# Kernel tuning notes

Measured on AMD Instinct MI355X. Metric: run time of the kernel, lower is better.

The kernel has to match this reference:

```python
import jax, jax.numpy as jnp
import numpy as np
from jax import lax

ORI = 256.0  # original image size hardcoded in feature_align
CIN  = [3, 64, 64, 128, 128, 256, 256, 256, 512, 512, 512]
COUT = [64, 64, 128, 128, 256, 256, 256, 512, 512, 512, 512]


def _conv(x, w, b):
    y = lax.conv_general_dilated(x, w, (1, 1), 'SAME',
                                 dimension_numbers=('NCHW', 'OIHW', 'NCHW'))
    return y + b[None, :, None, None]


def _pool(x):
    return lax.reduce_window(x, -jnp.inf, lax.max, (1, 1, 2, 2), (1, 1, 2, 2), 'VALID')


def _vgg(x, ws, bs):
    cr = lambda h, i: jax.nn.relu(_conv(h, ws[i], bs[i]))
    h = cr(x, 0); h = cr(h, 1); h = _pool(h)          # block1
    h = cr(h, 2); h = cr(h, 3); h = _pool(h)          # block2
    h = cr(h, 4); h = cr(h, 5); h = cr(h, 6); h = _pool(h)  # block3
    h = cr(h, 7); h = cr(h, 8); F = h                 # idx 20: relu(conv4_2)
    h = cr(h, 9); h = _pool(h)                        # conv4_3 + pool4
    U = cr(h, 10)                                     # idx 25: relu(conv5_1)
    return F, U


def _interp(im, px, py):
    # im: [C,H,W]; px,py: [n] point coords in original 256x256 space
    C, H, W = im.shape
    step = ORI / H  # feature maps are square (H==W)
    x = (px - step / 2) / ORI * H
    y = (py - step / 2) / ORI * W
    x0f = jnp.floor(x); y0f = jnp.floor(y)
    x0 = jnp.clip(x0f, 0, W - 1).astype(jnp.int32)
    x1 = jnp.clip(x0f + 1, 0, W - 1).astype(jnp.int32)
    y0 = jnp.clip(y0f, 0, H - 1).astype(jnp.int32)
    y1 = jnp.clip(y0f + 1, 0, H - 1).astype(jnp.int32)
    Ia = im[:, y0, x0]; Ib = im[:, y1, x0]; Ic = im[:, y0, x1]; Id = im[:, y1, x1]  # [C,n]
    # boundary weight adjustment, faithful to original scalar code
    xe = x0 == x1; ye = y0 == y1
    x0w = jnp.where(xe & (x0 == 0), x0 - 1, x0).astype(im.dtype)
    x1w = jnp.where(xe & (x0 != 0), x1 + 1, x1).astype(im.dtype)
    y0w = jnp.where(ye & (y0 == 0), y0 - 1, y0).astype(im.dtype)
    y1w = jnp.where(ye & (y0 != 0), y1 + 1, y1).astype(im.dtype)
    wa = (x1w - x) * (y1w - y); wb = (x1w - x) * (y - y0w)
    wc = (x - x0w) * (y1w - y); wd = (x - x0w) * (y - y0w)
    return Ia * wa + Ib * wb + Ic * wc + Id * wd  # [C,n]


def _feature_align(feat, P, mask):
    ns = jnp.sum(mask, axis=1)  # [B] valid point counts
    out = jax.vmap(_interp)(feat, P[..., 0], P[..., 1])  # [B,C,n]
    valid = (jnp.arange(P.shape[1])[None, :] < ns[:, None]).astype(feat.dtype)
    return out * valid[:, None, :]


def setup_inputs() -> dict:
    key = jax.random.key(0)
    ks = jax.random.split(key, 3 + 2 * len(CIN))
    inp = {
        'x': jax.random.normal(ks[0], (8, 3, 256, 256), dtype=jnp.float32),
        'points': jax.random.uniform(ks[1], (8, 32, 2), dtype=jnp.float32,
                                     minval=0.0, maxval=256.0),
        'mask': jnp.ones((8, 32), dtype=jnp.int32),
    }
    for i, (ci, co) in enumerate(zip(CIN, COUT)):
        std = np.sqrt(2.0 / (ci * 9))
        inp[f'w{i}'] = jax.random.normal(ks[2 + 2 * i], (co, ci, 3, 3), dtype=jnp.float32) * std
        inp[f'b{i}'] = jax.random.normal(ks[3 + 2 * i], (co,), dtype=jnp.float32) * 0.01
    return inp


def reference(x, points, mask,
              w0, b0, w1, b1, w2, b2, w3, b3, w4, b4, w5, b5,
              w6, b6, w7, b7, w8, b8, w9, b9, w10, b10):
    ws = [w0, w1, w2, w3, w4, w5, w6, w7, w8, w9, w10]
    bs = [b0, b1, b2, b3, b4, b5, b6, b7, b8, b9, b10]
    Fmap, Umap = _vgg(x, ws, bs)
    F = _feature_align(Fmap, points, mask)  # [B,512,n]
    U = _feature_align(Umap, points, mask)
    return F.transpose(0, 2, 1), U.transpose(0, 2, 1)
```

## Files before the change

### kernel.cpp

```cpp
#include <hip/hip_runtime.h>
#include <cstdint>

template <int CIS, int COB>
__global__ __launch_bounds__(256, 4) void conv1_k(
    const float* __restrict__ in, const float* __restrict__ wgt,
    const float* __restrict__ bias, float* __restrict__ out,
    int Cin, int Cout, int H, int W)
{
    const int tilesX = W >> 4;
    const int tx = blockIdx.x % tilesX;
    const int ty = blockIdx.x / tilesX;
    const int x0 = tx << 4, y0 = ty << 4;
    const int co0 = blockIdx.y * COB;
    const int n = blockIdx.z;
    in  += (size_t)n * Cin * H * W;
    out += (size_t)n * Cout * H * W;

    __shared__ float tile[CIS][18][20];
    __shared__ float wlds[CIS][COB][12];

    const int tid = threadIdx.x;
    const int lx = tid & 15, ly = tid >> 4;
    const int ox = x0 + lx, oy = y0 + ly;

    float acc[COB];
#pragma unroll
    for (int i = 0; i < COB; ++i) acc[i] = 0.f;

    for (int ci0 = 0; ci0 < Cin; ci0 += CIS) {
        for (int t = tid; t < CIS * 324; t += 256) {
            int s = t / 324;
            int rem = t - s * 324;
            int r = rem / 18, c = rem - r * 18;
            int gy = y0 - 1 + r, gx = x0 - 1 + c;
            const float* ip = in + (size_t)(ci0 + s) * H * W;
            float v = 0.f;
            if (gy >= 0 && gy < H && gx >= 0 && gx < W) v = ip[(size_t)gy * W + gx];
            tile[s][r][c] = v;
        }
        for (int t = tid; t < CIS * COB * 9; t += 256) {
            int co = t / (CIS * 9);
            int r  = t - co * (CIS * 9);
            int s  = r / 9, k = r - s * 9;
            wlds[s][co][k] = wgt[((size_t)(co0 + co) * Cin + (ci0 + s)) * 9 + k];
        }
        __syncthreads();
#pragma unroll
        for (int s = 0; s < CIS; ++s) {
            float p[3][3];
#pragma unroll
            for (int r = 0; r < 3; ++r)
#pragma unroll
                for (int c = 0; c < 3; ++c)
                    p[r][c] = tile[s][ly + r][lx + c];
#pragma unroll
            for (int co = 0; co < COB; ++co) {
                float wr[9];
#pragma unroll
                for (int k = 0; k < 9; ++k) wr[k] = wlds[s][co][k];
#pragma unroll
                for (int k = 0; k < 9; ++k)
                    acc[co] = fmaf(p[k / 3][k % 3], wr[k], acc[co]);
            }
        }
        __syncthreads();
    }
#pragma unroll
    for (int co = 0; co < COB; ++co) {
        float v = acc[co] + bias[co0 + co];
        v = v > 0.f ? v : 0.f;
        out[(size_t)(co0 + co) * H * W + (size_t)oy * W + ox] = v;
    }
}

template <int COB>
__global__ __launch_bounds__(256, 4) void conv2x2_k(
    const float* __restrict__ in, const float* __restrict__ wgt,
    const float* __restrict__ bias, float* __restrict__ out,
    int Cin, int Cout, int H, int W)
{
    const int tilesX = W >> 5;
    const int tx = blockIdx.x % tilesX;
    const int ty = blockIdx.x / tilesX;
    const int x0 = tx << 5, y0 = ty << 5;
    const int co0 = blockIdx.y * COB;
    const int n = blockIdx.z;
    in  += (size_t)n * Cin * H * W;
    out += (size_t)n * Cout * H * W;

    __shared__ float tile[4][34][36];
    __shared__ float wlds[4][COB][12];

    const int tid = threadIdx.x;
    const int lx = tid & 15, ly = tid >> 4;
    const int oy = y0 + 2 * ly, ox = x0 + 2 * lx;

    float acc[COB][2][2];
#pragma unroll
    for (int co = 0; co < COB; ++co)
#pragma unroll
        for (int dy = 0; dy < 2; ++dy)
#pragma unroll
            for (int dx = 0; dx < 2; ++dx) acc[co][dy][dx] = 0.f;

    for (int ci0 = 0; ci0 < Cin; ci0 += 4) {
        for (int t = tid; t < 4 * 1156; t += 256) {
            int s = t / 1156;
            int rem = t - s * 1156;
            int r = rem / 34, c = rem - r * 34;
            int gy = y0 - 1 + r, gx = x0 - 1 + c;
            const float* ip = in + (size_t)(ci0 + s) * H * W;
            float v = 0.f;
            if (gy >= 0 && gy < H && gx >= 0 && gx < W) v = ip[(size_t)gy * W + gx];
            tile[s][r][c] = v;
        }
        for (int t = tid; t < 4 * COB * 9; t += 256) {
            int co = t / 36;
            int r  = t - co * 36;
            int s  = r / 9, k = r - s * 9;
            wlds[s][co][k] = wgt[((size_t)(co0 + co) * Cin + (ci0 + s)) * 9 + k];
        }
        __syncthreads();
#pragma unroll
        for (int s = 0; s < 4; ++s) {
            float patch[4][4];
#pragma unroll
            for (int r = 0; r < 4; ++r) {
                const float* row = &tile[s][2 * ly + r][2 * lx];
#pragma unroll
                for (int c = 0; c < 4; ++c) patch[r][c] = row[c];
            }
#pragma unroll
            for (int co = 0; co < COB; ++co) {
                float wr[9];
#pragma unroll
                for (int k = 0; k < 9; ++k) wr[k] = wlds[s][co][k];
#pragma unroll
                for (int kr = 0; kr < 3; ++kr)
#pragma unroll
                    for (int kc = 0; kc < 3; ++kc) {
                        float wv = wr[kr * 3 + kc];
                        acc[co][0][0] = fmaf(patch[kr][kc],         wv, acc[co][0][0]);
                        acc[co][0][1] = fmaf(patch[kr][kc + 1],     wv, acc[co][0][1]);
                        acc[co][1][0] = fmaf(patch[kr + 1][kc],     wv, acc[co][1][0]);
                        acc[co][1][1] = fmaf(patch[kr + 1][kc + 1], wv, acc[co][1][1]);
                    }
            }
        }
        __syncthreads();
    }
#pragma unroll
    for (int co = 0; co < COB; ++co) {
        float bv = bias[co0 + co];
        float* op = out + (size_t)(co0 + co) * H * W + (size_t)oy * W + ox;
#pragma unroll
        for (int dy = 0; dy < 2; ++dy) {
            float v0 = acc[co][dy][0] + bv; v0 = v0 > 0.f ? v0 : 0.f;
            float v1 = acc[co][dy][1] + bv; v1 = v1 > 0.f ? v1 : 0.f;
            *reinterpret_cast<float2*>(op + (size_t)dy * W) = make_float2(v0, v1);
        }
    }
}

__global__ __launch_bounds__(256) void maxpool2x2_k(
    const float* __restrict__ in, float* __restrict__ out, int wshift)
{
    const int W = 1 << wshift, Wo = W >> 1;
    const int c = blockIdx.y;
    const int p = blockIdx.x * 256 + threadIdx.x;
    const int yo = p >> (wshift - 1);
    const int xo = p & (Wo - 1);
    const float* ip = in + ((size_t)c << (2 * wshift)) + (size_t)(2 * yo) * W + 2 * xo;
    float v0 = fmaxf(ip[0], ip[1]);
    float v1 = fmaxf(ip[W], ip[W + 1]);
    out[((size_t)c << (2 * wshift - 2)) + p] = fmaxf(v0, v1);
}

__global__ __launch_bounds__(256) void align_k(
    const float* __restrict__ feat, const float* __restrict__ pts,
    const int* __restrict__ mask, float* __restrict__ out,
    int B, int C, int H, int P)
{
    const int p = blockIdx.x, b = blockIdx.y;
    const int W = H;
    int ns = 0;
    for (int i = 0; i < P; ++i) ns += mask[b * P + i];
    const float valid = (p < ns) ? 1.f : 0.f;
    const float px = pts[((size_t)b * P + p) * 2 + 0];
    const float py = pts[((size_t)b * P + p) * 2 + 1];
    const float step = 256.0f / (float)H;
    const float x = (px - step * 0.5f) / 256.0f * (float)H;
    const float y = (py - step * 0.5f) / 256.0f * (float)W;
    const float x0f = floorf(x), y0f = floorf(y);
    const int x0 = min(max((int)x0f, 0), W - 1);
    const int x1 = min(max((int)x0f + 1, 0), W - 1);
    const int y0 = min(max((int)y0f, 0), H - 1);
    const int y1 = min(max((int)y0f + 1, 0), H - 1);
    const bool xe = (x0 == x1), ye = (y0 == y1);
    const float x0w = (xe && x0 == 0) ? -1.f : (float)x0;
    const float x1w = (xe && x0 != 0) ? (float)(x1 + 1) : (float)x1;
    const float y0w = (ye && y0 == 0) ? -1.f : (float)y0;
    const float y1w = (ye && y0 != 0) ? (float)(y1 + 1) : (float)y1;
    const float wa = (x1w - x) * (y1w - y);
    const float wb = (x1w - x) * (y - y0w);
    const float wc = (x - x0w) * (y1w - y);
    const float wd = (x - x0w) * (y - y0w);
    const float* f = feat + (size_t)b * C * H * W;
    for (int c = threadIdx.x; c < C; c += blockDim.x) {
        const float* fc = f + (size_t)c * H * W;
        float Ia = fc[y0 * W + x0];
        float Ib = fc[y1 * W + x0];
        float Ic = fc[y0 * W + x1];
        float Id = fc[y1 * W + x1];
        float v = Ia * wa + Ib * wb + Ic * wc + Id * wd;
        out[((size_t)b * P + p) * C + c] = v * valid;
    }
}

static inline void conv_auto(const float* in, const float* w, const float* b,
                             float* out, int N, int Cin, int Cout, int H,
                             hipStream_t s)
{
    if (Cin == 3) {
        int t = H >> 4;
        conv1_k<3, 8><<<dim3(t * t, Cout / 8, N), 256, 0, s>>>(in, w, b, out, Cin, Cout, H, H);
    } else if (H >= 64) {
        int t = H >> 5;
        conv2x2_k<8><<<dim3(t * t, Cout / 8, N), 256, 0, s>>>(in, w, b, out, Cin, Cout, H, H);
    } else {
        int t = H >> 4;
        conv1_k<4, 8><<<dim3(t * t, Cout / 8, N), 256, 0, s>>>(in, w, b, out, Cin, Cout, H, H);
    }
}

static inline void launch_pool(const float* in, float* out, int Ct, int H,
                               hipStream_t s)
{
    int wshift = 31 - __builtin_clz((unsigned)H);
    int pixels = (H >> 1) * (H >> 1);
    dim3 g((pixels + 255) / 256, Ct);
    maxpool2x2_k<<<g, 256, 0, s>>>(in, out, wshift);
}

extern "C" void kernel_launch(void* const* d_in, const int* in_sizes, int n_in,
                              void* d_out, int out_size, void* d_ws, size_t ws_size,
                              hipStream_t stream)
{
    const float* x   = (const float*)d_in[0];
    const float* pts = (const float*)d_in[1];
    const int*   msk = (const int*)d_in[2];
    const float* w[11]; const float* bb[11];
    for (int i = 0; i < 11; ++i) {
        w[i]  = (const float*)d_in[3 + 2 * i];
        bb[i] = (const float*)d_in[4 + 2 * i];
    }
    float* out = (float*)d_out;
    float* ws = (float*)d_ws;

    const size_t TA_FLOATS = 8388608ull + 4194304ull + 8388608ull;

    const float* Fmap; const float* Umap;

    if (ws_size >= TA_FLOATS * 4) {
        float* A  = ws;
        float* B  = A + 8388608;
        float* C  = B + 4194304;
        float* C0 = C;
        float* C1 = C + 4194304;

        for (int n = 0; n < 8; ++n) {
            const float* xn = x + (size_t)n * 3 * 65536;
            conv_auto(xn, w[0], bb[0], C0, 1, 3, 64, 256, stream);
            conv_auto(C0, w[1], bb[1], C1, 1, 64, 64, 256, stream);
            launch_pool(C1, A + (size_t)n * 64 * 16384, 64, 256, stream);
        }
        for (int g = 0; g < 4; ++g) {
            const float* src = A + (size_t)g * 2 * 64 * 16384;
            conv_auto(src, w[2], bb[2], C0, 2, 64, 128, 128, stream);
            conv_auto(C0,  w[3], bb[3], C1, 2, 128, 128, 128, stream);
            launch_pool(C1, B + (size_t)g * 2 * 128 * 4096, 2 * 128, 128, stream);
        }
        conv_auto(B, w[4], bb[4], A, 8, 128, 256, 64, stream);
        conv_auto(A, w[5], bb[5], C, 8, 256, 256, 64, stream);
        conv_auto(C, w[6], bb[6], A, 8, 256, 256, 64, stream);
        launch_pool(A, C, 8 * 256, 64, stream);
        conv_auto(C, w[7], bb[7], A, 8, 256, 512, 32, stream);
        conv_auto(A, w[8], bb[8], B, 8, 512, 512, 32, stream);
        conv_auto(B, w[9], bb[9], A, 8, 512, 512, 32, stream);
        launch_pool(A, C, 8 * 512, 32, stream);
        conv_auto(C, w[10], bb[10], A, 8, 512, 512, 16, stream);
        Fmap = B; Umap = A;
    } else {
        float* p0 = ws;
        float* p1 = p0 + 4194304;
        float* F  = p1 + 4194304;
        float* U  = F + 4194304;
        for (int n = 0; n < 8; ++n) {
            const float* xn = x + (size_t)n * 3 * 65536;
            float* Fn = F + (size_t)n * 512 * 1024;
            float* Un = U + (size_t)n * 512 * 256;
            conv_auto(xn, w[0], bb[0], p0, 1, 3, 64, 256, stream);
            conv_auto(p0, w[1], bb[1], p1, 1, 64, 64, 256, stream);
            launch_pool(p1, p0, 64, 256, stream);
            conv_auto(p0, w[2], bb[2], p1, 1, 64, 128, 128, stream);
            conv_auto(p1, w[3], bb[3], p0, 1, 128, 128, 128, stream);
            launch_pool(p0, p1, 128, 128, stream);
            conv_auto(p1, w[4], bb[4], p0, 1, 128, 256, 64, stream);
            conv_auto(p0, w[5], bb[5], p1, 1, 256, 256, 64, stream);
            conv_auto(p1, w[6], bb[6], p0, 1, 256, 256, 64, stream);
            launch_pool(p0, p1, 256, 64, stream);
            conv_auto(p1, w[7], bb[7], p0, 1, 256, 512, 32, stream);
            conv_auto(p0, w[8], bb[8], Fn, 1, 512, 512, 32, stream);
            conv_auto(Fn, w[9], bb[9], p0, 1, 512, 512, 32, stream);
            launch_pool(p0, p1, 512, 32, stream);
            conv_auto(p1, w[10], bb[10], Un, 1, 512, 512, 16, stream);
        }
        Fmap = F; Umap = U;
    }

    dim3 g(32, 8);
    align_k<<<g, 256, 0, stream>>>(Fmap, pts, msk, out,          8, 512, 32, 32);
    align_k<<<g, 256, 0, stream>>>(Umap, pts, msk, out + 131072, 8, 512, 16, 32);
}
```

Before: 9.996 ms.

## Read conv weights directly from global memory and retune conv kernel dispatch

Both direct-convolution kernels no longer stage weights in shared memory. They read them straight from global memory through uniform addresses, so the compiler can emit scalar loads. This removes the LDS staging loop and the per-iteration LDS weight reads. Separately, 32x32 layers are routed to the 2x2-output kernel, and conv layer 6 uses a 16-output-channel variant with a lowered occupancy bound. The cost is that each inner step now depends on global/scalar-cache load latency, and the larger COB raises register pressure.

```diff
diff --git a/kernel.cpp b/kernel.cpp
--- a/kernel.cpp
+++ b/kernel.cpp
@@ -17,7 +17,6 @@
     out += (size_t)n * Cout * H * W;
 
     __shared__ float tile[CIS][18][20];
-    __shared__ float wlds[CIS][COB][12];
 
     const int tid = threadIdx.x;
     const int lx = tid & 15, ly = tid >> 4;
@@ -38,12 +37,6 @@
             if (gy >= 0 && gy < H && gx >= 0 && gx < W) v = ip[(size_t)gy * W + gx];
             tile[s][r][c] = v;
         }
-        for (int t = tid; t < CIS * COB * 9; t += 256) {
-            int co = t / (CIS * 9);
-            int r  = t - co * (CIS * 9);
-            int s  = r / 9, k = r - s * 9;
-            wlds[s][co][k] = wgt[((size_t)(co0 + co) * Cin + (ci0 + s)) * 9 + k];
-        }
         __syncthreads();
 #pragma unroll
         for (int s = 0; s < CIS; ++s) {
@@ -55,12 +48,10 @@
                     p[r][c] = tile[s][ly + r][lx + c];
 #pragma unroll
             for (int co = 0; co < COB; ++co) {
-                float wr[9];
-#pragma unroll
-                for (int k = 0; k < 9; ++k) wr[k] = wlds[s][co][k];
+                const float* wc = wgt + ((size_t)(co0 + co) * Cin + (ci0 + s)) * 9;
 #pragma unroll
                 for (int k = 0; k < 9; ++k)
-                    acc[co] = fmaf(p[k / 3][k % 3], wr[k], acc[co]);
+                    acc[co] = fmaf(p[k / 3][k % 3], wc[k], acc[co]);
             }
         }
         __syncthreads();
@@ -74,7 +65,7 @@
 }
 
 template <int COB>
-__global__ __launch_bounds__(256, 4) void conv2x2_k(
+__global__ __launch_bounds__(256, (COB == 16 ? 2 : 4)) void conv2x2_k(
     const float* __restrict__ in, const float* __restrict__ wgt,
     const float* __restrict__ bias, float* __restrict__ out,
     int Cin, int Cout, int H, int W)
@@ -89,7 +80,6 @@
     out += (size_t)n * Cout * H * W;
 
     __shared__ float tile[4][34][36];
-    __shared__ float wlds[4][COB][12];
 
     const int tid = threadIdx.x;
     const int lx = tid & 15, ly = tid >> 4;
@@ -114,12 +104,6 @@
             if (gy >= 0 && gy < H && gx >= 0 && gx < W) v = ip[(size_t)gy * W + gx];
             tile[s][r][c] = v;
         }
-        for (int t = tid; t < 4 * COB * 9; t += 256) {
-            int co = t / 36;
-            int r  = t - co * 36;
-            int s  = r / 9, k = r - s * 9;
-            wlds[s][co][k] = wgt[((size_t)(co0 + co) * Cin + (ci0 + s)) * 9 + k];
-        }
         __syncthreads();
 #pragma unroll
         for (int s = 0; s < 4; ++s) {
@@ -132,14 +116,12 @@
             }
 #pragma unroll
             for (int co = 0; co < COB; ++co) {
-                float wr[9];
-#pragma unroll
-                for (int k = 0; k < 9; ++k) wr[k] = wlds[s][co][k];
+                const float* wc = wgt + ((size_t)(co0 + co) * Cin + (ci0 + s)) * 9;
 #pragma unroll
                 for (int kr = 0; kr < 3; ++kr)
 #pragma unroll
                     for (int kc = 0; kc < 3; ++kc) {
-                        float wv = wr[kr * 3 + kc];
+                        float wv = wc[kr * 3 + kc];
                         acc[co][0][0] = fmaf(patch[kr][kc],         wv, acc[co][0][0]);
                         acc[co][0][1] = fmaf(patch[kr][kc + 1],     wv, acc[co][0][1]);
                         acc[co][1][0] = fmaf(patch[kr + 1][kc],     wv, acc[co][1][0]);
@@ -224,7 +206,7 @@
     if (Cin == 3) {
         int t = H >> 4;
         conv1_k<3, 8><<<dim3(t * t, Cout / 8, N), 256, 0, s>>>(in, w, b, out, Cin, Cout, H, H);
-    } else if (H >= 64) {
+    } else if (H >= 32) {
         int t = H >> 5;
         conv2x2_k<8><<<dim3(t * t, Cout / 8, N), 256, 0, s>>>(in, w, b, out, Cin, Cout, H, H);
     } else {
@@ -282,7 +264,7 @@
         }
         conv_auto(B, w[4], bb[4], A, 8, 128, 256, 64, stream);
         conv_auto(A, w[5], bb[5], C, 8, 256, 256, 64, stream);
-        conv_auto(C, w[6], bb[6], A, 8, 256, 256, 64, stream);
+        conv2x2_k<16><<<dim3(4, 256 / 16, 8), 256, 0, stream>>>(C, w[6], bb[6], A, 256, 256, 64, 64);
         launch_pool(A, C, 8 * 256, 64, stream);
         conv_auto(C, w[7], bb[7], A, 8, 256, 512, 32, stream);
         conv_auto(A, w[8], bb[8], B, 8, 512, 512, 32, stream);
```

Result: slower. 10.75 ms (+7.5%).
